# Optimization experiments

Hardware: AMD Instinct MI355X
Metric: run time of the kernel (lower is better)

## Reference

```python
import math
import jax, jax.numpy as jnp
import numpy as np

B, S, D, H = 2, 2048, 2048, 16
HD = D // H  # 128


def _rope_tables(seq_len, head_dim, theta=10000.0):
    freqs = 1.0 / (theta ** (np.arange(0, head_dim, 2, dtype=np.float32) / head_dim))
    t = np.arange(seq_len, dtype=np.float32)
    ang = np.outer(t, freqs)  # [S, HD/2]
    return jnp.asarray(np.cos(ang)), jnp.asarray(np.sin(ang))


def setup_inputs() -> dict:
    key = jax.random.key(0)
    ks = jax.random.split(key, 5)
    sc = 1.0 / math.sqrt(D)
    x = jax.random.normal(ks[0], (B, S, D), dtype=jnp.float32)
    wq = jax.random.normal(ks[1], (D, D), dtype=jnp.float32) * sc
    wk = jax.random.normal(ks[2], (D, D), dtype=jnp.float32) * sc
    wv = jax.random.normal(ks[3], (D, D), dtype=jnp.float32) * sc
    wo = jax.random.normal(ks[4], (D, D), dtype=jnp.float32) * sc
    freqs_cos, freqs_sin = _rope_tables(S, HD)
    # additive causal mask: 0 on/below diagonal, -inf above
    mask = jnp.where(jnp.tril(jnp.ones((S, S), dtype=bool)), 0.0, -jnp.inf).astype(jnp.float32)
    return {"x": x, "wq": wq, "wk": wk, "wv": wv, "wo": wo,
            "freqs_cos": freqs_cos, "freqs_sin": freqs_sin,
            "mask": mask, "start_pos": 0}


def _apply_rope(t, cos, sin):
    # t: [B, S, H, HD]; pairs (even, odd) rotated as complex numbers (LLaMA style)
    tr = t.reshape(*t.shape[:-1], HD // 2, 2)
    te, to = tr[..., 0], tr[..., 1]
    c = cos[None, :, None, :]
    s = sin[None, :, None, :]
    out_e = te * c - to * s
    out_o = te * s + to * c
    return jnp.stack([out_e, out_o], axis=-1).reshape(t.shape)


def reference(x, wq, wk, wv, wo, freqs_cos, freqs_sin, mask, start_pos):
    bsz, seqlen, _ = x.shape
    xq = (x @ wq.T).reshape(bsz, seqlen, H, HD)
    xk = (x @ wk.T).reshape(bsz, seqlen, H, HD)
    xv = (x @ wv.T).reshape(bsz, seqlen, H, HD)
    xq = _apply_rope(xq, freqs_cos, freqs_sin)
    xk = _apply_rope(xk, freqs_cos, freqs_sin)
    # n_rep == 1 so repeat_kv is identity
    scores = jnp.einsum('bqhd,bkhd->bhqk', xq, xk) / math.sqrt(HD)
    scores = scores + mask  # broadcast [S,S] over [B,H,S,S]
    probs = jax.nn.softmax(scores.astype(jnp.float32), axis=-1).astype(xq.dtype)
    out = jnp.einsum('bhqk,bkhd->bqhd', probs, xv).reshape(bsz, seqlen, -1)
    return out @ wo.T
```

## Files before the change

### kernel.cpp

```cpp
#include <hip/hip_runtime.h>


typedef __bf16 bf16_t;
typedef __bf16 bf16x4 __attribute__((ext_vector_type(4)));
typedef __bf16 bf16x8 __attribute__((ext_vector_type(8)));
typedef float  f32x4  __attribute__((ext_vector_type(4)));

#define DEV __device__ __forceinline__

DEV void async_copy16(const bf16_t* g, bf16_t* lds_uniform_base) {
    __builtin_amdgcn_global_load_lds(
        (const __attribute__((address_space(1))) void*)g,
        (__attribute__((address_space(3))) void*)lds_uniform_base,
        16, 0, 0);
}

__global__ void cast_all(const float* __restrict__ x,  const float* __restrict__ wq,
                         const float* __restrict__ wk, const float* __restrict__ wv,
                         const float* __restrict__ wo,
                         bf16_t* __restrict__ xb, bf16_t* __restrict__ W3,
                         bf16_t* __restrict__ wob)
{
    const int i = blockIdx.x * blockDim.x + threadIdx.x;
    const float4* src;
    bf16x4* dst;
    if (i < 2097152) {
        src = (const float4*)x + i;
        dst = (bf16x4*)xb + i;
    } else {
        const int j   = i - 2097152;
        const int r   = j >> 20;
        const int off = j & 1048575;
        const float* s4 = (r == 0) ? wq : (r == 1) ? wk : (r == 2) ? wv : wo;
        src = (const float4*)s4 + off;
        dst = (r < 3) ? ((bf16x4*)W3 + (long)r * 1048576 + off)
                      : ((bf16x4*)wob + off);
    }
    const float4 v = *src;
    bf16x4 o = { (bf16_t)v.x, (bf16_t)v.y, (bf16_t)v.z, (bf16_t)v.w };
    *dst = o;
}

__global__ __launch_bounds__(256)
void gemm_qkv(const bf16_t* __restrict__ A, const bf16_t* __restrict__ Bm,
              bf16_t* __restrict__ Qo, bf16_t* __restrict__ Ko,
              bf16_t* __restrict__ VTo,
              const float* __restrict__ cosT, const float* __restrict__ sinT)
{
    constexpr int K = 2048;
    __shared__ bf16_t As[128 * 32];
    __shared__ bf16_t Bs[128 * 32];

    const int tid  = threadIdx.x;
    const int w    = tid >> 6;
    const int lane = tid & 63;
    const int l16  = lane & 15;
    const int quad = lane >> 4;
    const int wm   = w >> 1, wn = w & 1;

    const int id   = blockIdx.x;
    const int xcd  = id & 7;
    const int slot = id >> 3;
    const int nl   = slot % 6;
    const int ml   = slot / 6;
    const long n0  = (long)(xcd * 6 + nl) * 128;
    const long m0  = (long)ml * 128;

    f32x4 acc[4][4] = {};

    const int srow = tid >> 2;
    const int soff = (tid & 3) * 8;
    const bf16_t* Ag = A  + (m0 + srow) * K + soff;
    const bf16_t* Bg = Bm + (n0 + srow) * K + soff;

    for (int k0 = 0; k0 < K; k0 += 32) {
        __syncthreads();
        async_copy16(Ag + k0,          As + w * 512);
        async_copy16(Ag + 64 * K + k0, As + 2048 + w * 512);
        async_copy16(Bg + k0,          Bs + w * 512);
        async_copy16(Bg + 64 * K + k0, Bs + 2048 + w * 512);
        __syncthreads();

        bf16x8 af[4], bfr[4];
        #pragma unroll
        for (int t = 0; t < 4; ++t) {
            af[t]  = *(const bf16x8*)&As[(wm * 64 + t * 16 + l16) * 32 + quad * 8];
            bfr[t] = *(const bf16x8*)&Bs[(wn * 64 + t * 16 + l16) * 32 + quad * 8];
        }
        #pragma unroll
        for (int mt = 0; mt < 4; ++mt)
            #pragma unroll
            for (int nt = 0; nt < 4; ++nt)
                acc[mt][nt] = __builtin_amdgcn_mfma_f32_16x16x32_bf16(
                    af[mt], bfr[nt], acc[mt][nt], 0, 0, 0);
    }

    const int region = (int)(n0 >> 11);
    #pragma unroll
    for (int mt = 0; mt < 4; ++mt) {
        #pragma unroll
        for (int nt = 0; nt < 4; ++nt) {
            if (region < 2) {
                bf16_t* dst = (region == 0) ? Qo : Ko;
                #pragma unroll
                for (int r = 0; r < 4; ++r) {
                    const long m = m0 + wm * 64 + mt * 16 + quad * 4 + r;
                    const long n = n0 + wn * 64 + nt * 16 + l16;
                    float v = acc[mt][nt][r];
                    const float partner = __shfl_xor(v, 1);
                    const int d    = (int)n & 127;
                    const int fidx = ((int)m & 2047) * 64 + (d >> 1);
                    const float c = cosT[fidx], s = sinT[fidx];
                    v = ((int)n & 1) ? fmaf(partner, s, v * c)
                                     : (v * c - partner * s);
                    dst[m * 2048 + (n & 2047)] = (bf16_t)v;
                }
            } else {
                const long m  = m0 + wm * 64 + mt * 16 + quad * 4;
                const int  np = (int)(n0 + wn * 64 + nt * 16 + l16) - 4096;
                bf16x4 pk;
                #pragma unroll
                for (int r = 0; r < 4; ++r) pk[r] = (bf16_t)acc[mt][nt][r];
                const int b  = (int)(m >> 11);
                const int s0 = (int)m & 2047;
                const long idx = ((long)(b * 16 + (np >> 7)) * 128 + (np & 127)) * 2048 + s0;
                *(bf16x4*)&VTo[idx] = pk;
            }
        }
    }
}

__global__ __launch_bounds__(256)
void gemm_out(const bf16_t* __restrict__ A, const bf16_t* __restrict__ Bm,
              float* __restrict__ Cp)
{
    constexpr int K = 2048, N = 2048;
    __shared__ bf16_t As[128 * 32];
    __shared__ bf16_t Bs[128 * 32];

    const int tid  = threadIdx.x;
    const int w    = tid >> 6;
    const int lane = tid & 63;
    const int l16  = lane & 15;
    const int quad = lane >> 4;
    const int wm   = w >> 1, wn = w & 1;

    const int id   = blockIdx.x;
    const int xcd  = id & 7;
    const int slot = id >> 3;
    const long n0  = (long)(xcd * 2 + (slot & 1)) * 128;
    const long m0  = (long)(slot >> 1) * 128;

    f32x4 acc[4][4] = {};

    const int srow = tid >> 2;
    const int soff = (tid & 3) * 8;
    const bf16_t* Ag = A  + (m0 + srow) * K + soff;
    const bf16_t* Bg = Bm + (n0 + srow) * K + soff;

    for (int k0 = 0; k0 < K; k0 += 32) {
        __syncthreads();
        async_copy16(Ag + k0,          As + w * 512);
        async_copy16(Ag + 64 * K + k0, As + 2048 + w * 512);
        async_copy16(Bg + k0,          Bs + w * 512);
        async_copy16(Bg + 64 * K + k0, Bs + 2048 + w * 512);
        __syncthreads();

        bf16x8 af[4], bfr[4];
        #pragma unroll
        for (int t = 0; t < 4; ++t) {
            af[t]  = *(const bf16x8*)&As[(wm * 64 + t * 16 + l16) * 32 + quad * 8];
            bfr[t] = *(const bf16x8*)&Bs[(wn * 64 + t * 16 + l16) * 32 + quad * 8];
        }
        #pragma unroll
        for (int mt = 0; mt < 4; ++mt)
            #pragma unroll
            for (int nt = 0; nt < 4; ++nt)
                acc[mt][nt] = __builtin_amdgcn_mfma_f32_16x16x32_bf16(
                    af[mt], bfr[nt], acc[mt][nt], 0, 0, 0);
    }

    #pragma unroll
    for (int mt = 0; mt < 4; ++mt)
        #pragma unroll
        for (int nt = 0; nt < 4; ++nt)
            #pragma unroll
            for (int r = 0; r < 4; ++r) {
                const long m = m0 + wm * 64 + mt * 16 + quad * 4 + r;
                const long n = n0 + wn * 64 + nt * 16 + l16;
                Cp[m * N + n] = acc[mt][nt][r];
            }
}

__global__ __launch_bounds__(256, 2)
void flash_attn(const bf16_t* __restrict__ Q, const bf16_t* __restrict__ Kg,
                const bf16_t* __restrict__ VT, bf16_t* __restrict__ O)
{
    constexpr int S = 2048, D = 2048;
    constexpr int PSTR = 72;
    __shared__ bf16_t Kb[2][64 * 128];
    __shared__ bf16_t Vb[128 * 64];
    __shared__ bf16_t Ps[128 * PSTR];

    const int tid  = threadIdx.x;
    const int w    = tid >> 6, lane = tid & 63, l16 = lane & 15, quad = lane >> 4;
    const int l7   = l16 & 7;

    const int id   = blockIdx.x;
    const int half = id >> 8;
    const int rest = id & 255;
    const int xcd  = rest & 7;
    const int s    = rest >> 3;
    const int hh   = s & 3;
    const int qh   = s >> 2;
    const int qt   = half ? (15 - qh) : qh;
    const int bh   = xcd * 4 + hh;
    const int b    = bh >> 4, h = bh & 15;
    const int q0   = qt * 128;

    bf16x8 qf[2][4];
    {
        const bf16_t* qp = Q + (long)(b * S + q0 + w * 32 + l16) * D + h * 128 + quad * 8;
        #pragma unroll
        for (int qi = 0; qi < 2; ++qi)
            #pragma unroll
            for (int kk = 0; kk < 4; ++kk)
                qf[qi][kk] = *(const bf16x8*)(qp + qi * 16 * D + kk * 32);
    }

    int koff[4], vof[4];
    #pragma unroll
    for (int i = 0; i < 4; ++i) {
        const int c  = i * 256 + tid;
        const int kr = c >> 4, cs = c & 15;
        const int cc = (cs & 8) | ((cs & 7) ^ (kr & 7));
        koff[i] = kr * D + cc * 8;
        const int d  = c >> 3, vs = c & 7;
        vof[i] = d * S + (vs ^ (d & 7)) * 8;
    }
    const bf16_t* Kst = Kg + (long)b * S * D + h * 128;
    const bf16_t* Vst = VT + (long)bh * 128 * S;

    f32x4 oacc[2][8] = {};
    float li[2] = { 0.f, 0.f };
    const float SC = 0.08838834764831845f * 1.44269504088896340f;

    const int nkt = 2 * qt + 2;

    #pragma unroll
    for (int i = 0; i < 4; ++i)
        async_copy16(Kst + koff[i], &Kb[0][i * 2048 + w * 512]);

    for (int kt = 0; kt < nkt; ++kt) {
        __syncthreads();
        {
            const bf16_t* vp = Vst + kt * 64;
            const bf16_t* kp = Kst + (long)(kt + 1) * 64 * D;
            #pragma unroll
            for (int i = 0; i < 4; ++i) {
                async_copy16(vp + vof[i], &Vb[i * 2048 + w * 512]);
                async_copy16(kp + koff[i], &Kb[(kt + 1) & 1][i * 2048 + w * 512]);
            }
        }

        const bool active = (kt * 64 <= q0 + w * 32 + 31);
        if (active) {
            f32x4 sc[4][2] = {};
            const bf16_t* Kcur = Kb[kt & 1];
            #pragma unroll
            for (int kk = 0; kk < 4; ++kk)
                #pragma unroll
                for (int mt = 0; mt < 4; ++mt) {
                    const int cc = kk * 4 + quad;
                    const bf16x8 kf = *(const bf16x8*)
                        &Kcur[(mt * 16 + l16) * 128 + ((cc & 8) | ((cc & 7) ^ l7)) * 8];
                    sc[mt][0] = __builtin_amdgcn_mfma_f32_16x16x32_bf16(
                        kf, qf[0][kk], sc[mt][0], 0, 0, 0);
                    sc[mt][1] = __builtin_amdgcn_mfma_f32_16x16x32_bf16(
                        kf, qf[1][kk], sc[mt][1], 0, 0, 0);
                }

            #pragma unroll
            for (int qi = 0; qi < 2; ++qi) {
                const int qg = q0 + w * 32 + qi * 16 + l16;
                float rs = 0.f;
                #pragma unroll
                for (int mt = 0; mt < 4; ++mt) {
                    bf16x4 pk;
                    #pragma unroll
                    for (int r = 0; r < 4; ++r) {
                        const int kg = kt * 64 + mt * 16 + quad * 4 + r;
                        const float p = (kg > qg) ? 0.f
                                      : exp2f(sc[mt][qi][r] * SC - 24.0f);
                        rs += p;
                        pk[r] = (bf16_t)p;
                    }
                    *(bf16x4*)&Ps[(w * 32 + qi * 16 + l16) * PSTR + mt * 16 + quad * 4] = pk;
                }
                li[qi] += rs;
            }
        }

        __syncthreads();

        if (active) {
            #pragma unroll
            for (int ks = 0; ks < 2; ++ks) {
                const bf16x8 pf0 = *(const bf16x8*)
                    &Ps[(w * 32 + l16) * PSTR + ks * 32 + quad * 8];
                const bf16x8 pf1 = *(const bf16x8*)
                    &Ps[(w * 32 + 16 + l16) * PSTR + ks * 32 + quad * 8];
                #pragma unroll
                for (int nv = 0; nv < 8; ++nv) {
                    const bf16x8 vf = *(const bf16x8*)
                        &Vb[(nv * 16 + l16) * 64 + ((ks * 4 + quad) ^ l7) * 8];
                    oacc[0][nv] = __builtin_amdgcn_mfma_f32_16x16x32_bf16(
                        pf0, vf, oacc[0][nv], 0, 0, 0);
                    oacc[1][nv] = __builtin_amdgcn_mfma_f32_16x16x32_bf16(
                        pf1, vf, oacc[1][nv], 0, 0, 0);
                }
            }
        }
    }

    #pragma unroll
    for (int qi = 0; qi < 2; ++qi) {
        li[qi] += __shfl_xor(li[qi], 16);
        li[qi] += __shfl_xor(li[qi], 32);
        const float inv = 1.0f / li[qi];
        #pragma unroll
        for (int r = 0; r < 4; ++r) {
            const float invr = __shfl(inv, quad * 4 + r);
            const long  row  = (long)(b * S + q0 + w * 32 + qi * 16 + quad * 4 + r);
            #pragma unroll
            for (int nv = 0; nv < 8; ++nv)
                O[row * D + h * 128 + nv * 16 + l16] = (bf16_t)(oacc[qi][nv][r] * invr);
        }
    }
}

extern "C" void kernel_launch(void* const* d_in, const int* in_sizes, int n_in,
                              void* d_out, int out_size, void* d_ws, size_t ws_size,
                              hipStream_t stream) {
    const float* x  = (const float*)d_in[0];
    const float* wq = (const float*)d_in[1];
    const float* wk = (const float*)d_in[2];
    const float* wv = (const float*)d_in[3];
    const float* wo = (const float*)d_in[4];
    const float* fc = (const float*)d_in[5];
    const float* fs = (const float*)d_in[6];

    char* ws = (char*)d_ws;
    bf16_t* xb  = (bf16_t*)(ws + 0);
    bf16_t* W3  = (bf16_t*)(ws + (16l << 20));
    bf16_t* wob = (bf16_t*)(ws + (40l << 20));
    bf16_t* Qb  = (bf16_t*)(ws + (48l << 20));
    bf16_t* Kb  = (bf16_t*)(ws + (64l << 20));
    bf16_t* VTb = (bf16_t*)(ws + (80l << 20));
    bf16_t* Ob  = xb;

    cast_all<<<24576, 256, 0, stream>>>(x, wq, wk, wv, wo, xb, W3, wob);

    gemm_qkv<<<1536, 256, 0, stream>>>(xb, W3, Qb, Kb, VTb, fc, fs);

    flash_attn<<<512, 256, 0, stream>>>(Qb, Kb, VTb, Ob);

    gemm_out<<<512, 256, 0, stream>>>(Ob, wob, (float*)d_out);
}
```

Baseline: 423.6 us.

## Deepen GEMM K-tiles with swizzled LDS and stream V through registers

Both projection GEMMs now stage 64-wide K tiles per barrier pair instead of 32, using an XOR-swizzled LDS layout. This halves the number of sync rounds and is meant to reduce LDS bank conflicts. Flash attention no longer stages V in LDS. Each lane loads its V fragments from global memory straight into registers, prefetching the next tile while the current one feeds MFMAs, which removes the V LDS buffer and one barrier per iteration. In exchange, register pressure rises by 64 VGPRs per thread, and the V reads are strided, uncoalesced global loads that depend on cache behaviour.

```diff
diff --git a/kernel.cpp b/kernel.cpp
--- a/kernel.cpp
+++ b/kernel.cpp
@@ -48,14 +48,15 @@
               const float* __restrict__ cosT, const float* __restrict__ sinT)
 {
     constexpr int K = 2048;
-    __shared__ bf16_t As[128 * 32];
-    __shared__ bf16_t Bs[128 * 32];
+    __shared__ bf16_t As[128 * 64];
+    __shared__ bf16_t Bs[128 * 64];
 
     const int tid  = threadIdx.x;
     const int w    = tid >> 6;
     const int lane = tid & 63;
     const int l16  = lane & 15;
     const int quad = lane >> 4;
+    const int l7   = l16 & 7;
     const int wm   = w >> 1, wn = w & 1;
 
     const int id   = blockIdx.x;
@@ -68,31 +69,42 @@
 
     f32x4 acc[4][4] = {};
 
-    const int srow = tid >> 2;
-    const int soff = (tid & 3) * 8;
-    const bf16_t* Ag = A  + (m0 + srow) * K + soff;
-    const bf16_t* Bg = Bm + (n0 + srow) * K + soff;
-
-    for (int k0 = 0; k0 < K; k0 += 32) {
-        __syncthreads();
-        async_copy16(Ag + k0,          As + w * 512);
-        async_copy16(Ag + 64 * K + k0, As + 2048 + w * 512);
-        async_copy16(Bg + k0,          Bs + w * 512);
-        async_copy16(Bg + 64 * K + k0, Bs + 2048 + w * 512);
-        __syncthreads();
-
-        bf16x8 af[4], bfr[4];
-        #pragma unroll
-        for (int t = 0; t < 4; ++t) {
-            af[t]  = *(const bf16x8*)&As[(wm * 64 + t * 16 + l16) * 32 + quad * 8];
-            bfr[t] = *(const bf16x8*)&Bs[(wn * 64 + t * 16 + l16) * 32 + quad * 8];
-        }
-        #pragma unroll
-        for (int mt = 0; mt < 4; ++mt)
-            #pragma unroll
-            for (int nt = 0; nt < 4; ++nt)
-                acc[mt][nt] = __builtin_amdgcn_mfma_f32_16x16x32_bf16(
-                    af[mt], bfr[nt], acc[mt][nt], 0, 0, 0);
+    const bf16_t* Ag[4];
+    const bf16_t* Bg[4];
+    #pragma unroll
+    for (int i = 0; i < 4; ++i) {
+        const int c   = i * 256 + tid;
+        const int row = c >> 3;
+        const int col = ((c & 7) ^ (row & 7)) * 8;
+        Ag[i] = A  + (m0 + row) * K + col;
+        Bg[i] = Bm + (n0 + row) * K + col;
+    }
+
+    for (int k0 = 0; k0 < K; k0 += 64) {
+        __syncthreads();
+        #pragma unroll
+        for (int i = 0; i < 4; ++i) {
+            async_copy16(Ag[i] + k0, As + i * 2048 + w * 512);
+            async_copy16(Bg[i] + k0, Bs + i * 2048 + w * 512);
+        }
+        __syncthreads();
+
+        #pragma unroll
+        for (int kc = 0; kc < 2; ++kc) {
+            bf16x8 af[4], bfr[4];
+            #pragma unroll
+            for (int t = 0; t < 4; ++t) {
+                const int cs = ((kc * 4 + quad) ^ l7) * 8;
+                af[t]  = *(const bf16x8*)&As[(wm * 64 + t * 16 + l16) * 64 + cs];
+                bfr[t] = *(const bf16x8*)&Bs[(wn * 64 + t * 16 + l16) * 64 + cs];
+            }
+            #pragma unroll
+            for (int mt = 0; mt < 4; ++mt)
+                #pragma unroll
+                for (int nt = 0; nt < 4; ++nt)
+                    acc[mt][nt] = __builtin_amdgcn_mfma_f32_16x16x32_bf16(
+                        af[mt], bfr[nt], acc[mt][nt], 0, 0, 0);
+        }
     }
 
     const int region = (int)(n0 >> 11);
@@ -135,14 +147,15 @@
               float* __restrict__ Cp)
 {
     constexpr int K = 2048, N = 2048;
-    __shared__ bf16_t As[128 * 32];
-    __shared__ bf16_t Bs[128 * 32];
+    __shared__ bf16_t As[128 * 64];
+    __shared__ bf16_t Bs[128 * 64];
 
     const int tid  = threadIdx.x;
     const int w    = tid >> 6;
     const int lane = tid & 63;
     const int l16  = lane & 15;
     const int quad = lane >> 4;
+    const int l7   = l16 & 7;
     const int wm   = w >> 1, wn = w & 1;
 
     const int id   = blockIdx.x;
@@ -153,31 +166,42 @@
 
     f32x4 acc[4][4] = {};
 
-    const int srow = tid >> 2;
-    const int soff = (tid & 3) * 8;
-    const bf16_t* Ag = A  + (m0 + srow) * K + soff;
-    const bf16_t* Bg = Bm + (n0 + srow) * K + soff;
-
-    for (int k0 = 0; k0 < K; k0 += 32) {
-        __syncthreads();
-        async_copy16(Ag + k0,          As + w * 512);
-        async_copy16(Ag + 64 * K + k0, As + 2048 + w * 512);
-        async_copy16(Bg + k0,          Bs + w * 512);
-        async_copy16(Bg + 64 * K + k0, Bs + 2048 + w * 512);
-        __syncthreads();
-
-        bf16x8 af[4], bfr[4];
-        #pragma unroll
-        for (int t = 0; t < 4; ++t) {
-            af[t]  = *(const bf16x8*)&As[(wm * 64 + t * 16 + l16) * 32 + quad * 8];
-            bfr[t] = *(const bf16x8*)&Bs[(wn * 64 + t * 16 + l16) * 32 + quad * 8];
-        }
-        #pragma unroll
-        for (int mt = 0; mt < 4; ++mt)
-            #pragma unroll
-            for (int nt = 0; nt < 4; ++nt)
-                acc[mt][nt] = __builtin_amdgcn_mfma_f32_16x16x32_bf16(
-                    af[mt], bfr[nt], acc[mt][nt], 0, 0, 0);
+    const bf16_t* Ag[4];
+    const bf16_t* Bg[4];
+    #pragma unroll
+    for (int i = 0; i < 4; ++i) {
+        const int c   = i * 256 + tid;
+        const int row = c >> 3;
+        const int col = ((c & 7) ^ (row & 7)) * 8;
+        Ag[i] = A  + (m0 + row) * K + col;
+        Bg[i] = Bm + (n0 + row) * K + col;
+    }
+
+    for (int k0 = 0; k0 < K; k0 += 64) {
+        __syncthreads();
+        #pragma unroll
+        for (int i = 0; i < 4; ++i) {
+            async_copy16(Ag[i] + k0, As + i * 2048 + w * 512);
+            async_copy16(Bg[i] + k0, Bs + i * 2048 + w * 512);
+        }
+        __syncthreads();
+
+        #pragma unroll
+        for (int kc = 0; kc < 2; ++kc) {
+            bf16x8 af[4], bfr[4];
+            #pragma unroll
+            for (int t = 0; t < 4; ++t) {
+                const int cs = ((kc * 4 + quad) ^ l7) * 8;
+                af[t]  = *(const bf16x8*)&As[(wm * 64 + t * 16 + l16) * 64 + cs];
+                bfr[t] = *(const bf16x8*)&Bs[(wn * 64 + t * 16 + l16) * 64 + cs];
+            }
+            #pragma unroll
+            for (int mt = 0; mt < 4; ++mt)
+                #pragma unroll
+                for (int nt = 0; nt < 4; ++nt)
+                    acc[mt][nt] = __builtin_amdgcn_mfma_f32_16x16x32_bf16(
+                        af[mt], bfr[nt], acc[mt][nt], 0, 0, 0);
+        }
     }
 
     #pragma unroll
@@ -199,7 +223,6 @@
     constexpr int S = 2048, D = 2048;
     constexpr int PSTR = 72;
     __shared__ bf16_t Kb[2][64 * 128];
-    __shared__ bf16_t Vb[128 * 64];
     __shared__ bf16_t Ps[128 * PSTR];
 
     const int tid  = threadIdx.x;
@@ -228,18 +251,16 @@
                 qf[qi][kk] = *(const bf16x8*)(qp + qi * 16 * D + kk * 32);
     }
 
-    int koff[4], vof[4];
+    int koff[4];
     #pragma unroll
     for (int i = 0; i < 4; ++i) {
         const int c  = i * 256 + tid;
         const int kr = c >> 4, cs = c & 15;
         const int cc = (cs & 8) | ((cs & 7) ^ (kr & 7));
         koff[i] = kr * D + cc * 8;
-        const int d  = c >> 3, vs = c & 7;
-        vof[i] = d * S + (vs ^ (d & 7)) * 8;
     }
     const bf16_t* Kst = Kg + (long)b * S * D + h * 128;
-    const bf16_t* Vst = VT + (long)bh * 128 * S;
+    const bf16_t* Vl  = VT + (long)bh * 128 * S + (long)l16 * S + quad * 8;
 
     f32x4 oacc[2][8] = {};
     float li[2] = { 0.f, 0.f };
@@ -250,18 +271,20 @@
     #pragma unroll
     for (int i = 0; i < 4; ++i)
         async_copy16(Kst + koff[i], &Kb[0][i * 2048 + w * 512]);
+    bf16x8 vf[2][8];
+    #pragma unroll
+    for (int ks = 0; ks < 2; ++ks)
+        #pragma unroll
+        for (int nv = 0; nv < 8; ++nv)
+            vf[ks][nv] = *(const bf16x8*)(Vl + (long)nv * 16 * S + ks * 32);
 
     for (int kt = 0; kt < nkt; ++kt) {
         __syncthreads();
-        {
-            const bf16_t* vp = Vst + kt * 64;
-            const bf16_t* kp = Kst + (long)(kt + 1) * 64 * D;
-            #pragma unroll
-            for (int i = 0; i < 4; ++i) {
-                async_copy16(vp + vof[i], &Vb[i * 2048 + w * 512]);
-                async_copy16(kp + koff[i], &Kb[(kt + 1) & 1][i * 2048 + w * 512]);
-            }
-        }
+        const int knx = (kt + 1 < nkt) ? (kt + 1) : kt;
+        #pragma unroll
+        for (int i = 0; i < 4; ++i)
+            async_copy16(Kst + (long)knx * 64 * D + koff[i],
+                         &Kb[(kt + 1) & 1][i * 2048 + w * 512]);
 
         const bool active = (kt * 64 <= q0 + w * 32 + 31);
         if (active) {
@@ -299,11 +322,7 @@
                 }
                 li[qi] += rs;
             }
-        }
-
-        __syncthreads();
-
-        if (active) {
+
             #pragma unroll
             for (int ks = 0; ks < 2; ++ks) {
                 const bf16x8 pf0 = *(const bf16x8*)
@@ -312,12 +331,13 @@
                     &Ps[(w * 32 + 16 + l16) * PSTR + ks * 32 + quad * 8];
                 #pragma unroll
                 for (int nv = 0; nv < 8; ++nv) {
-                    const bf16x8 vf = *(const bf16x8*)
-                        &Vb[(nv * 16 + l16) * 64 + ((ks * 4 + quad) ^ l7) * 8];
+                    const bf16x8 vcur = vf[ks][nv];
+                    vf[ks][nv] = *(const bf16x8*)
+                        (Vl + (long)nv * 16 * S + ks * 32 + (long)knx * 64);
                     oacc[0][nv] = __builtin_amdgcn_mfma_f32_16x16x32_bf16(
-                        pf0, vf, oacc[0][nv], 0, 0, 0);
+                        pf0, vcur, oacc[0][nv], 0, 0, 0);
                     oacc[1][nv] = __builtin_amdgcn_mfma_f32_16x16x32_bf16(
-                        pf1, vf, oacc[1][nv], 0, 0, 0);
+                        pf1, vcur, oacc[1][nv], 0, 0, 0);
                 }
             }
         }
```

After: 431.4 us. Within noise of the previous version (+1.8%).

## Deepen QKV GEMM k-tile with swizzled LDS and double-buffer V in attention

Applied to the files above, without the earlier changes.

The QKV GEMM now loads 64-wide k-tiles into XOR-swizzled LDS, which halves the barrier count per k and avoids bank conflicts on the fragment reads. The flash attention kernel double-buffers V alongside K, prefetching the next tile. This removes the mid-iteration barrier between softmax and PV, since each wave only reads its own P rows. The cost is more LDS per block, which may limit occupancy. The loads are also still synchronous within each GEMM iteration, so no real overlap is added there.

```diff
diff --git a/kernel.cpp b/kernel.cpp
--- a/kernel.cpp
+++ b/kernel.cpp
@@ -48,14 +48,15 @@
               const float* __restrict__ cosT, const float* __restrict__ sinT)
 {
     constexpr int K = 2048;
-    __shared__ bf16_t As[128 * 32];
-    __shared__ bf16_t Bs[128 * 32];
+    __shared__ bf16_t As[128 * 64];
+    __shared__ bf16_t Bs[128 * 64];
 
     const int tid  = threadIdx.x;
     const int w    = tid >> 6;
     const int lane = tid & 63;
     const int l16  = lane & 15;
     const int quad = lane >> 4;
+    const int l7   = l16 & 7;
     const int wm   = w >> 1, wn = w & 1;
 
     const int id   = blockIdx.x;
@@ -68,31 +69,42 @@
 
     f32x4 acc[4][4] = {};
 
-    const int srow = tid >> 2;
-    const int soff = (tid & 3) * 8;
-    const bf16_t* Ag = A  + (m0 + srow) * K + soff;
-    const bf16_t* Bg = Bm + (n0 + srow) * K + soff;
-
-    for (int k0 = 0; k0 < K; k0 += 32) {
-        __syncthreads();
-        async_copy16(Ag + k0,          As + w * 512);
-        async_copy16(Ag + 64 * K + k0, As + 2048 + w * 512);
-        async_copy16(Bg + k0,          Bs + w * 512);
-        async_copy16(Bg + 64 * K + k0, Bs + 2048 + w * 512);
-        __syncthreads();
-
-        bf16x8 af[4], bfr[4];
-        #pragma unroll
-        for (int t = 0; t < 4; ++t) {
-            af[t]  = *(const bf16x8*)&As[(wm * 64 + t * 16 + l16) * 32 + quad * 8];
-            bfr[t] = *(const bf16x8*)&Bs[(wn * 64 + t * 16 + l16) * 32 + quad * 8];
-        }
-        #pragma unroll
-        for (int mt = 0; mt < 4; ++mt)
-            #pragma unroll
-            for (int nt = 0; nt < 4; ++nt)
-                acc[mt][nt] = __builtin_amdgcn_mfma_f32_16x16x32_bf16(
-                    af[mt], bfr[nt], acc[mt][nt], 0, 0, 0);
+    const bf16_t* Ag[4];
+    const bf16_t* Bg[4];
+    #pragma unroll
+    for (int i = 0; i < 4; ++i) {
+        const int c   = i * 256 + tid;
+        const int row = c >> 3;
+        const int col = ((c & 7) ^ (row & 7)) * 8;
+        Ag[i] = A  + (m0 + row) * K + col;
+        Bg[i] = Bm + (n0 + row) * K + col;
+    }
+
+    for (int k0 = 0; k0 < K; k0 += 64) {
+        __syncthreads();
+        #pragma unroll
+        for (int i = 0; i < 4; ++i) {
+            async_copy16(Ag[i] + k0, As + i * 2048 + w * 512);
+            async_copy16(Bg[i] + k0, Bs + i * 2048 + w * 512);
+        }
+        __syncthreads();
+
+        #pragma unroll
+        for (int kc = 0; kc < 2; ++kc) {
+            bf16x8 af[4], bfr[4];
+            #pragma unroll
+            for (int t = 0; t < 4; ++t) {
+                const int cs = ((kc * 4 + quad) ^ l7) * 8;
+                af[t]  = *(const bf16x8*)&As[(wm * 64 + t * 16 + l16) * 64 + cs];
+                bfr[t] = *(const bf16x8*)&Bs[(wn * 64 + t * 16 + l16) * 64 + cs];
+            }
+            #pragma unroll
+            for (int mt = 0; mt < 4; ++mt)
+                #pragma unroll
+                for (int nt = 0; nt < 4; ++nt)
+                    acc[mt][nt] = __builtin_amdgcn_mfma_f32_16x16x32_bf16(
+                        af[mt], bfr[nt], acc[mt][nt], 0, 0, 0);
+        }
     }
 
     const int region = (int)(n0 >> 11);
@@ -199,7 +211,7 @@
     constexpr int S = 2048, D = 2048;
     constexpr int PSTR = 72;
     __shared__ bf16_t Kb[2][64 * 128];
-    __shared__ bf16_t Vb[128 * 64];
+    __shared__ bf16_t Vb[2][128 * 64];
     __shared__ bf16_t Ps[128 * PSTR];
 
     const int tid  = threadIdx.x;
@@ -248,19 +260,20 @@
     const int nkt = 2 * qt + 2;
 
     #pragma unroll
-    for (int i = 0; i < 4; ++i)
+    for (int i = 0; i < 4; ++i) {
         async_copy16(Kst + koff[i], &Kb[0][i * 2048 + w * 512]);
+        async_copy16(Vst + vof[i], &Vb[0][i * 2048 + w * 512]);
+    }
 
     for (int kt = 0; kt < nkt; ++kt) {
         __syncthreads();
-        {
-            const bf16_t* vp = Vst + kt * 64;
-            const bf16_t* kp = Kst + (long)(kt + 1) * 64 * D;
-            #pragma unroll
-            for (int i = 0; i < 4; ++i) {
-                async_copy16(vp + vof[i], &Vb[i * 2048 + w * 512]);
-                async_copy16(kp + koff[i], &Kb[(kt + 1) & 1][i * 2048 + w * 512]);
-            }
+        const int nk = (kt + 1 < nkt) ? kt + 1 : kt;
+        #pragma unroll
+        for (int i = 0; i < 4; ++i) {
+            async_copy16(Kst + (long)nk * 64 * D + koff[i],
+                         &Kb[(kt + 1) & 1][i * 2048 + w * 512]);
+            async_copy16(Vst + (long)nk * 64 + vof[i],
+                         &Vb[(kt + 1) & 1][i * 2048 + w * 512]);
         }
 
         const bool active = (kt * 64 <= q0 + w * 32 + 31);
@@ -299,11 +312,8 @@
                 }
                 li[qi] += rs;
             }
-        }
-
-        __syncthreads();
-
-        if (active) {
+
+            const bf16_t* Vcur = Vb[kt & 1];
             #pragma unroll
             for (int ks = 0; ks < 2; ++ks) {
                 const bf16x8 pf0 = *(const bf16x8*)
@@ -313,7 +323,7 @@
                 #pragma unroll
                 for (int nv = 0; nv < 8; ++nv) {
                     const bf16x8 vf = *(const bf16x8*)
-                        &Vb[(nv * 16 + l16) * 64 + ((ks * 4 + quad) ^ l7) * 8];
+                        &Vcur[(nv * 16 + l16) * 64 + ((ks * 4 + quad) ^ l7) * 8];
                     oacc[0][nv] = __builtin_amdgcn_mfma_f32_16x16x32_bf16(
                         pf0, vf, oacc[0][nv], 0, 0, 0);
                     oacc[1][nv] = __builtin_amdgcn_mfma_f32_16x16x32_bf16(
```

Result: faster. 399.3 us (-5.7%).
